# Performance work log

Hardware: AMD Instinct MI355X
Metric: run time of the kernel (lower is better)

## Reference

```python
import jax, jax.numpy as jnp
import numpy as np

N = 8192
H_DIM = 128
N_CLASSES = 10


def _cdist(a, b):
    # Euclidean distance matrix, torch.cdist(p=2) equivalent.
    d2 = (jnp.sum(a * a, axis=1)[:, None]
          + jnp.sum(b * b, axis=1)[None, :]
          - 2.0 * (a @ b.T))
    return jnp.sqrt(jnp.maximum(d2, 0.0))


def _adagae_regularization(distances, k):
    # Per-row sort-based adaptive-kernel thresholding (AdaGAE).
    sd = jnp.sort(distances, axis=1)            # [n, n]
    a = sd[:, k][:, None] + 1e-10               # k-th NN distance per row
    b = jnp.sum(sd[:, :k], axis=1)[:, None]     # sum of k nearest
    c = jax.nn.relu(a - distances)
    denom = a * k - b + 1e-10
    out = c / denom
    return (out + out.T) / 2.0


def _get_kernel(x, ohm_labels, sparsity):
    unknown = jnp.sum(ohm_labels, axis=1) == 0   # [n] bool
    known = ~unknown
    kk = known[:, None] & known[None, :]         # known-known region
    uu = unknown[:, None] & unknown[None, :]     # unknown-unknown region
    semantic = ohm_labels @ ohm_labels.T
    ed = _cdist(x, x)
    ed = (ed + ed.T) / 2.0
    adagae = _adagae_regularization(ed, sparsity)
    n_unknown = jnp.sum(unknown.astype(jnp.float32))
    fc = 1.0 / jnp.maximum(n_unknown, 1.0)       # heterogeneous fully-connected value
    kernel = jnp.where(kk, semantic, jnp.where(uu, adagae, fc))
    return kernel


def setup_inputs() -> dict:
    key = jax.random.key(0)
    k1, k2, k3 = jax.random.split(key, 3)
    x = jax.random.normal(k1, (N, H_DIM), dtype=jnp.float32)
    # labels in [0, N_CLASSES]; label == N_CLASSES -> unknown (all-zero one-hot row)
    labels = jax.random.randint(k2, (N,), 0, N_CLASSES + 1)
    ohm_labels = jnp.where((labels < N_CLASSES)[:, None],
                           jax.nn.one_hot(labels, N_CLASSES, dtype=jnp.float32),
                           0.0)
    W = jax.random.normal(k3, (2, H_DIM), dtype=jnp.float32) / np.sqrt(H_DIM)
    b = jnp.zeros((2,), dtype=jnp.float32)
    return {"x": x, "ohm_labels": ohm_labels, "W": W, "b": b, "spars": 32}


def reference(x, ohm_labels, W, b, spars):
    adj = _get_kernel(x, ohm_labels, spars)      # [n, n]
    h = x @ W.T + b                              # [n, 2]
    g = jnp.tanh(adj @ h)                        # [n, 2]
    # centroids (missing clusters stay zero)
    counts = jnp.sum(ohm_labels, axis=0)         # [n_classes]
    agg = ohm_labels.T @ g                       # [n_classes, 2]
    centroids = jnp.where((counts > 0)[:, None],
                          agg / jnp.maximum(counts, 1.0)[:, None], 0.0)
    scores = -_cdist(g, centroids)               # [n, n_classes]
    return scores, g, adj
```

## Files before the change

kernel.cpp:

```cpp
#include <hip/hip_runtime.h>
#include <hip/hip_bf16.h>
#include <math.h>

#define N 8192
#define D 128
#define NC 10

typedef float f4 __attribute__((ext_vector_type(4)));

__device__ __forceinline__ void nt_store4(float* p, float a, float b, float c, float d) {
    f4 v; v[0] = a; v[1] = b; v[2] = c; v[3] = d;
    __builtin_nontemporal_store(v, (f4*)p);
}


__global__ void k_zero(int* __restrict__ p) {
    if (threadIdx.x == 0) *p = 0;
}

__global__ void k_prep(const float* __restrict__ x, const float* __restrict__ ohm,
                       const float* __restrict__ W, const float* __restrict__ bb,
                       char* __restrict__ labs, float* __restrict__ nArr,
                       float* __restrict__ h, int* __restrict__ u_idx,
                       int* __restrict__ cpos, int* __restrict__ nuCnt) {
    int gt = blockIdx.x * blockDim.x + threadIdx.x;
    int wid = gt >> 6;
    int lane = gt & 63;
    if (wid >= N) return;
    const float2* xr = (const float2*)(x + (size_t)wid * D);
    float2 xv = xr[lane];
    float2 w0 = ((const float2*)W)[lane];
    float2 w1 = ((const float2*)(W + D))[lane];
    float nn = xv.x * xv.x + xv.y * xv.y;
    float h0 = xv.x * w0.x + xv.y * w0.y;
    float h1 = xv.x * w1.x + xv.y * w1.y;
    for (int off = 32; off; off >>= 1) {
        nn += __shfl_down(nn, off);
        h0 += __shfl_down(h0, off);
        h1 += __shfl_down(h1, off);
    }
    if (lane == 0) {
        nArr[wid] = nn;
        h[wid * 2 + 0] = h0 + bb[0];
        h[wid * 2 + 1] = h1 + bb[1];
        const float* orow = ohm + (size_t)wid * NC;
        int lab = -1;
        for (int c = 0; c < NC; ++c) {
            if (orow[c] > 0.5f) { lab = c; break; }
        }
        labs[wid] = (char)lab;
        if (lab < 0) {
            int slot = atomicAdd(nuCnt, 1);
            u_idx[slot] = wid;
            cpos[wid] = slot;
        }
    }
}

__global__ void k_sumA(const char* __restrict__ labs, const float* __restrict__ h,
                       float* __restrict__ part1) {
    __shared__ float L[256][33];
    int t = threadIdx.x;
    for (int s = 0; s < 33; ++s) L[t][s] = 0.f;
    int row = blockIdx.x * 256 + t;
    if (row < N) {
        int lab = labs[row];
        float h0 = h[row * 2], h1 = h[row * 2 + 1];
        if (lab >= 0) {
            L[t][lab * 2] = h0; L[t][lab * 2 + 1] = h1; L[t][22 + lab] = 1.f;
        } else {
            L[t][20] = h0; L[t][21] = h1; L[t][32] = 1.f;
        }
    }
    __syncthreads();
    if (t < 33) {
        float s = 0.f;
        for (int i = 0; i < 256; ++i) s += L[i][t];
        part1[blockIdx.x * 33 + t] = s;
    }
}

__global__ void k_sumB(const float* __restrict__ part1, float* __restrict__ scal) {
    int t = threadIdx.x;
    if (t < 33) {
        float s = 0.f;
        for (int i = 0; i < 64; ++i) s += part1[i * 33 + t];
        scal[t] = s;
    }
    __syncthreads();
    if (t == 0) {
        scal[33] = 1.0f / fmaxf(scal[32], 1.0f);
    }
}

__global__ void k_gemm(const float* __restrict__ x, const float* __restrict__ nArr,
                       const int* __restrict__ u_idx, const int* __restrict__ nuCnt,
                       int cap, float* __restrict__ d2a, float* __restrict__ adj) {
    __shared__ float As[64][132];
    __shared__ float Bs[64][132];
    __shared__ int Ai[64];
    int nu = *nuCnt;
    float* dst = (nu <= cap) ? d2a : adj;
    int t = threadIdx.x;
    int j0 = blockIdx.x * 64;
    for (int yy = blockIdx.y; yy * 64 < nu && yy < 128; yy += 12) {
        int a0 = yy * 64;
        if (yy != (int)blockIdx.y) __syncthreads();
        for (int c = t; c < 64 * 32; c += 256) {
            int r = c >> 5, c4 = c & 31;
            int a = a0 + r;
            int orig = (a < nu) ? u_idx[a] : u_idx[0];
            if (c4 == 0) Ai[r] = (a < nu) ? orig : -1;
            float4 av = ((const float4*)(x + (size_t)orig * D))[c4];
            *(float4*)&As[r][c4 * 4] = av;
            float4 bv = ((const float4*)(x + (size_t)(j0 + r) * D))[c4];
            *(float4*)&Bs[r][c4 * 4] = bv;
        }
        __syncthreads();
        int tx = t & 15, ty = t >> 4;
        float acc[4][4];
#pragma unroll
        for (int m = 0; m < 4; ++m)
#pragma unroll
            for (int q = 0; q < 4; ++q) acc[m][q] = 0.f;
#pragma unroll 4
        for (int k4 = 0; k4 < 32; ++k4) {
            float4 a4[4], b4[4];
#pragma unroll
            for (int m = 0; m < 4; ++m) a4[m] = *(const float4*)&As[ty + 16 * m][k4 * 4];
#pragma unroll
            for (int q = 0; q < 4; ++q) b4[q] = *(const float4*)&Bs[tx + 16 * q][k4 * 4];
#pragma unroll
            for (int m = 0; m < 4; ++m)
#pragma unroll
                for (int q = 0; q < 4; ++q)
                    acc[m][q] += a4[m].x * b4[q].x + a4[m].y * b4[q].y
                               + a4[m].z * b4[q].z + a4[m].w * b4[q].w;
        }
#pragma unroll
        for (int m = 0; m < 4; ++m) {
            int ar = ty + 16 * m;
            int orig = Ai[ar];
            if (orig < 0) continue;
            float ni = nArr[orig];
#pragma unroll
            for (int q = 0; q < 4; ++q) {
                int j = j0 + tx + 16 * q;
                float v = fmaxf(ni + nArr[j] - 2.f * acc[m][q], 0.f);
                if (orig == j) v = 0.f;
                dst[(size_t)(a0 + ar) * N + j] = v;
            }
        }
    }
}

__global__ void k_self(const float* __restrict__ d2a, const float* __restrict__ adj_ro,
                       const int* __restrict__ u_idx, const int* __restrict__ nuCnt,
                       int cap, const int* __restrict__ spars,
                       const char* __restrict__ labs,
                       float* __restrict__ aArr, float* __restrict__ dinv,
                       float* __restrict__ adj) {
    __shared__ float wsf[4];
    __shared__ int wsi[8];
    int nu = *nuCnt;
    int t = threadIdx.x;
    int bid = blockIdx.x;
    if (bid >= 1024) {
        if (nu > cap) return;
        float fc = 1.0f / fmaxf((float)nu, 1.0f);
        int fb = bid - 1024;
        for (int rr = 0; rr < 4; ++rr) {
            int i = fb + 2048 * rr;
            int li = labs[i];
            if (li < 0) continue;
            float* row = adj + (size_t)i * N;
#pragma unroll
            for (int s = 0; s < 8; ++s) {
                int c4 = t + 256 * s;
                char4 l4 = ((const char4*)labs)[c4];
                float o0 = (l4.x < 0) ? fc : ((l4.x == li) ? 1.f : 0.f);
                float o1 = (l4.y < 0) ? fc : ((l4.y == li) ? 1.f : 0.f);
                float o2 = (l4.z < 0) ? fc : ((l4.z == li) ? 1.f : 0.f);
                float o3 = (l4.w < 0) ? fc : ((l4.w == li) ? 1.f : 0.f);
                nt_store4(row + c4 * 4, o0, o1, o2, o3);
            }
        }
        return;
    }
    const float* src = (nu <= cap) ? d2a : adj_ro;
    int k = *spars;
    int need = k + 1;
    int w = t >> 6;
    for (int rr = 0; rr < 8; ++rr) {
        int a = bid + 1024 * rr;
        if (a >= nu) break;
        const float4* rp = (const float4*)(src + (size_t)a * N);
        float v[32];
#pragma unroll
        for (int s = 0; s < 8; ++s) {
            float4 q = rp[t + 256 * s];
            v[s * 4 + 0] = q.x; v[s * 4 + 1] = q.y; v[s * 4 + 2] = q.z; v[s * 4 + 3] = q.w;
        }
        unsigned lo = 0u, hi = 0x7F800000u;
        for (int it = 0; it < 32; ++it) {
            unsigned mid = (lo + hi) >> 1;
            float mf = __uint_as_float(mid);
            int c = 0;
#pragma unroll
            for (int s = 0; s < 32; ++s) c += (v[s] <= mf) ? 1 : 0;
            for (int off = 32; off; off >>= 1) c += __shfl_down(c, off);
            if ((t & 63) == 0) wsi[(it & 1) * 4 + w] = c;
            __syncthreads();
            int base = (it & 1) * 4;
            c = wsi[base] + wsi[base + 1] + wsi[base + 2] + wsi[base + 3];
            if (lo < hi) {
                if (c >= need) hi = mid; else lo = mid + 1;
            }
        }
        float kvf = __uint_as_float(hi);
        float sum = 0.f; int clt = 0;
#pragma unroll
        for (int s = 0; s < 32; ++s) {
            if (v[s] < kvf) { clt++; sum += sqrtf(v[s]); }
        }
        for (int off = 32; off; off >>= 1) {
            sum += __shfl_down(sum, off);
            clt += __shfl_down(clt, off);
        }
        __syncthreads();
        if ((t & 63) == 0) { wsf[w] = sum; wsi[w] = clt; }
        __syncthreads();
        if (t == 0) {
            float sAll = wsf[0] + wsf[1] + wsf[2] + wsf[3];
            int cAll = wsi[0] + wsi[1] + wsi[2] + wsi[3];
            float skv = sqrtf(kvf);
            float aV = skv + 1e-10f;
            float b = sAll + (float)(k - cAll) * skv;
            float denom = aV * (float)k - b + 1e-10f;
            int orig = u_idx[a];
            aArr[orig] = aV;
            dinv[orig] = 1.0f / denom;
        }
        __syncthreads();
    }
}

__global__ void k_fu(const float* __restrict__ d2a, const char* __restrict__ labs,
                     const int* __restrict__ u_idx, const float* __restrict__ aArr,
                     const float* __restrict__ dinv, const float* __restrict__ h,
                     const int* __restrict__ nuCnt, int cap,
                     float* __restrict__ adj, float* __restrict__ gp) {
    __shared__ float red[256];
    int nu = *nuCnt;
    if (nu > cap) return;
    int t = threadIdx.x;
    int jc = blockIdx.x;
    float fc = 1.0f / fmaxf((float)nu, 1.0f);
    const float2* h2 = (const float2*)h;
    for (int a = blockIdx.y; a < nu; a += 768) {
        int i = u_idx[a];
        float ai = aArr[i], di = dinv[i];
        const float* drow = d2a + (size_t)a * N;
        float* orow = adj + (size_t)i * N;
        float s0 = 0.f, s1 = 0.f;
#pragma unroll
        for (int s = 0; s < 2; ++s) {
            int c4 = jc * 512 + s * 256 + t;
            int j = c4 * 4;
            float4 dv = ((const float4*)drow)[c4];
            char4 l4 = ((const char4*)labs)[c4];
            float dd[4] = {dv.x, dv.y, dv.z, dv.w};
            signed char ll[4] = {(signed char)l4.x, (signed char)l4.y,
                                 (signed char)l4.z, (signed char)l4.w};
            float v[4];
#pragma unroll
            for (int q = 0; q < 4; ++q) {
                if (ll[q] >= 0) {
                    v[q] = fc;
                } else {
                    float d = sqrtf(dd[q]);
                    v[q] = 0.5f * (fmaxf(ai - d, 0.f) * di
                                 + fmaxf(aArr[j + q] - d, 0.f) * dinv[j + q]);
                }
                float2 hh = h2[j + q];
                s0 += v[q] * hh.x;
                s1 += v[q] * hh.y;
            }
            nt_store4(orow + j, v[0], v[1], v[2], v[3]);
        }
        red[t] = s0; __syncthreads();
        for (int off = 128; off; off >>= 1) {
            if (t < off) red[t] += red[t + off];
            __syncthreads();
        }
        float r0 = red[0];
        __syncthreads();
        red[t] = s1; __syncthreads();
        for (int off = 128; off; off >>= 1) {
            if (t < off) red[t] += red[t + off];
            __syncthreads();
        }
        if (t == 0) { gp[a * 8 + jc * 2 + 0] = r0; gp[a * 8 + jc * 2 + 1] = red[0]; }
        __syncthreads();
    }
}

__global__ void k_fill_known_fb(const char* __restrict__ labs,
                                const int* __restrict__ nuCnt, int cap,
                                float* __restrict__ adj) {
    int nu = *nuCnt;
    if (nu <= cap) return;
    int t = threadIdx.x;
    float fc = 1.0f / fmaxf((float)nu, 1.0f);
    for (int rr = 0; rr < 4; ++rr) {
        int i = blockIdx.x + 2048 * rr;
        int li = labs[i];
        if (li < 0) continue;
        float* row = adj + (size_t)i * N;
#pragma unroll
        for (int s = 0; s < 8; ++s) {
            int c4 = t + 256 * s;
            char4 l4 = ((const char4*)labs)[c4];
            float o0 = (l4.x < 0) ? fc : ((l4.x == li) ? 1.f : 0.f);
            float o1 = (l4.y < 0) ? fc : ((l4.y == li) ? 1.f : 0.f);
            float o2 = (l4.z < 0) ? fc : ((l4.z == li) ? 1.f : 0.f);
            float o3 = (l4.w < 0) ? fc : ((l4.w == li) ? 1.f : 0.f);
            nt_store4(row + c4 * 4, o0, o1, o2, o3);
        }
    }
}

__global__ void k_fu_slow(const float* __restrict__ x, const float* __restrict__ nArr,
                          const int* __restrict__ u_idx, const int* __restrict__ nuCnt,
                          int cap, const char* __restrict__ labs,
                          const float* __restrict__ aArr, const float* __restrict__ dinv,
                          float* __restrict__ adj) {
    __shared__ float As[64][D + 1];
    __shared__ float Bs[64][D + 1];
    __shared__ int Ai[64];
    int nu = *nuCnt;
    if (nu <= cap) return;
    int t = threadIdx.x;
    float fc = 1.0f / fmaxf((float)nu, 1.0f);
    int j0 = blockIdx.x * 64;
    for (int yy = blockIdx.y; yy * 64 < nu && yy < 128; yy += 12) {
        int a0 = yy * 64;
        if (yy != (int)blockIdx.y) __syncthreads();
        for (int c = t; c < 64 * 32; c += 256) {
            int r = c >> 5, c4 = c & 31;
            int a = a0 + r;
            int orig = (a < nu) ? u_idx[a] : u_idx[0];
            if (c4 == 0) Ai[r] = (a < nu) ? orig : -1;
            float4 av = ((const float4*)(x + (size_t)orig * D))[c4];
            As[r][c4 * 4 + 0] = av.x; As[r][c4 * 4 + 1] = av.y;
            As[r][c4 * 4 + 2] = av.z; As[r][c4 * 4 + 3] = av.w;
            float4 bv = ((const float4*)(x + (size_t)(j0 + r) * D))[c4];
            Bs[r][c4 * 4 + 0] = bv.x; Bs[r][c4 * 4 + 1] = bv.y;
            Bs[r][c4 * 4 + 2] = bv.z; Bs[r][c4 * 4 + 3] = bv.w;
        }
        __syncthreads();
        int tx = t & 15, ty = t >> 4;
        float acc[4][4];
#pragma unroll
        for (int m = 0; m < 4; ++m)
#pragma unroll
            for (int q = 0; q < 4; ++q) acc[m][q] = 0.f;
#pragma unroll 4
        for (int k = 0; k < D; ++k) {
            float a4[4], b4[4];
#pragma unroll
            for (int m = 0; m < 4; ++m) a4[m] = As[ty * 4 + m][k];
#pragma unroll
            for (int q = 0; q < 4; ++q) b4[q] = Bs[tx * 4 + q][k];
#pragma unroll
            for (int m = 0; m < 4; ++m)
#pragma unroll
                for (int q = 0; q < 4; ++q) acc[m][q] += a4[m] * b4[q];
        }
#pragma unroll
        for (int m = 0; m < 4; ++m) {
            int ar = ty * 4 + m;
            int orig = Ai[ar];
            if (orig < 0) continue;
            float ni = nArr[orig];
            float ai = aArr[orig], di = dinv[orig];
            int jb = j0 + tx * 4;
            float4 o;
            float* op = (float*)&o;
#pragma unroll
            for (int q = 0; q < 4; ++q) {
                int j = jb + q;
                int lj = labs[j];
                float v;
                if (lj >= 0) {
                    v = fc;
                } else {
                    float d2 = fmaxf(ni + nArr[j] - 2.f * acc[m][q], 0.f);
                    if (orig == j) d2 = 0.f;
                    float d = sqrtf(d2);
                    v = 0.5f * (fmaxf(ai - d, 0.f) * di + fmaxf(aArr[j] - d, 0.f) * dinv[j]);
                }
                op[q] = v;
            }
            *((float4*)(adj + (size_t)orig * N + jb)) = o;
        }
    }
}

__global__ void k_gv(const float* __restrict__ adj, const float* __restrict__ h,
                     const int* __restrict__ u_idx, const int* __restrict__ nuCnt,
                     int cap, float* __restrict__ gpre) {
    __shared__ float red[256];
    int nu = *nuCnt;
    if (nu <= cap) return;
    int t = threadIdx.x;
    const float2* h2 = (const float2*)h;
    for (int rr = 0; rr < 8; ++rr) {
        int a = blockIdx.x + 1024 * rr;
        if (a >= nu) break;
        int orig = u_idx[a];
        const float4* row = (const float4*)(adj + (size_t)orig * N);
        float s0 = 0.f, s1 = 0.f;
#pragma unroll
        for (int s = 0; s < 8; ++s) {
            int c4 = t + 256 * s;
            float4 v = row[c4];
            int j = c4 * 4;
            float2 ha = h2[j + 0], hb = h2[j + 1], hc = h2[j + 2], hd = h2[j + 3];
            s0 += v.x * ha.x + v.y * hb.x + v.z * hc.x + v.w * hd.x;
            s1 += v.x * ha.y + v.y * hb.y + v.z * hc.y + v.w * hd.y;
        }
        red[t] = s0; __syncthreads();
        for (int off = 128; off; off >>= 1) {
            if (t < off) red[t] += red[t + off];
            __syncthreads();
        }
        if (t == 0) gpre[orig * 2 + 0] = red[0];
        __syncthreads();
        red[t] = s1; __syncthreads();
        for (int off = 128; off; off >>= 1) {
            if (t < off) red[t] += red[t + off];
            __syncthreads();
        }
        if (t == 0) gpre[orig * 2 + 1] = red[0];
        __syncthreads();
    }
}

__global__ void k_gagg(const char* __restrict__ labs, const float* __restrict__ gp,
                       const float* __restrict__ gpre, const int* __restrict__ cpos,
                       const int* __restrict__ nuCnt, int cap,
                       const float* __restrict__ scal, float* __restrict__ outg,
                       float* __restrict__ part2) {
    __shared__ float L[256][21];
    int nu = *nuCnt;
    int t = threadIdx.x;
    for (int s = 0; s < 20; ++s) L[t][s] = 0.f;
    int i = blockIdx.x * 256 + t;
    int li = labs[i];
    float fc = scal[33];
    float g0, g1;
    if (li >= 0) {
        g0 = scal[li * 2 + 0] + fc * scal[20];
        g1 = scal[li * 2 + 1] + fc * scal[21];
    } else if (nu <= cap) {
        int a = cpos[i];
        g0 = gp[a * 8 + 0] + gp[a * 8 + 2] + gp[a * 8 + 4] + gp[a * 8 + 6];
        g1 = gp[a * 8 + 1] + gp[a * 8 + 3] + gp[a * 8 + 5] + gp[a * 8 + 7];
    } else {
        g0 = gpre[i * 2 + 0];
        g1 = gpre[i * 2 + 1];
    }
    g0 = tanhf(g0); g1 = tanhf(g1);
    outg[i * 2 + 0] = g0;
    outg[i * 2 + 1] = g1;
    if (li >= 0) { L[t][li * 2 + 0] = g0; L[t][li * 2 + 1] = g1; }
    __syncthreads();
    if (t < 20) {
        float s = 0.f;
        for (int r = 0; r < 256; ++r) s += L[r][t];
        part2[blockIdx.x * 20 + t] = s;
    }
}

__global__ void k_scores(const float* __restrict__ g, const float* __restrict__ part2,
                         const float* __restrict__ scal, float* __restrict__ outs) {
    __shared__ float cent[20];
    int t = threadIdx.x;
    if (t < 20) {
        float s = 0.f;
        for (int i = 0; i < 32; ++i) s += part2[i * 20 + t];
        float cnt = scal[22 + (t >> 1)];
        cent[t] = (cnt > 0.f) ? s / fmaxf(cnt, 1.0f) : 0.f;
    }
    __syncthreads();
    int i = blockIdx.x * 256 + t;
    float g0 = g[i * 2 + 0], g1 = g[i * 2 + 1];
#pragma unroll
    for (int c = 0; c < NC; ++c) {
        float d0 = g0 - cent[c * 2 + 0];
        float d1 = g1 - cent[c * 2 + 1];
        outs[i * NC + c] = -sqrtf(d0 * d0 + d1 * d1);
    }
}

extern "C" void kernel_launch(void* const* d_in, const int* in_sizes, int n_in,
                              void* d_out, int out_size, void* d_ws, size_t ws_size,
                              hipStream_t stream) {
    const float* x = (const float*)d_in[0];
    const float* ohm = (const float*)d_in[1];
    const float* W = (const float*)d_in[2];
    const float* b = (const float*)d_in[3];
    const int* spars = (const int*)d_in[4];

    float* out = (float*)d_out;
    float* outScores = out;
    float* outG = out + (size_t)N * NC;
    float* adj = outG + (size_t)N * 2;

    char* wsb = (char*)d_ws;
    int* u_idx   = (int*)(wsb + 0);
    char* labs   = (char*)(wsb + 32768);
    float* nArr  = (float*)(wsb + 40960);
    float* aArr  = (float*)(wsb + 73728);
    float* dinv  = (float*)(wsb + 106496);
    float* hArr  = (float*)(wsb + 139264);
    float* gpre  = (float*)(wsb + 204800);
    float* part1 = (float*)(wsb + 270336);
    float* part2 = (float*)(wsb + 278784);
    float* scal  = (float*)(wsb + 283904);
    int* nuCnt   = (int*)(wsb + 284160);
    int* cpos    = (int*)(wsb + 335872);
    float* gp    = (float*)(wsb + 524288);
    float* d2a   = (float*)(wsb + 2097152);

    long capL = ((long)ws_size - 2097152L) / ((long)N * 4);
    if (capL < 0) capL = 0;
    if (capL > N) capL = N;
    int cap = (int)capL;
    bool mayFallback = (cap < N);

    k_zero<<<1, 64, 0, stream>>>(nuCnt);
    k_prep<<<2048, 256, 0, stream>>>(x, ohm, W, b, labs, nArr, hArr, u_idx, cpos, nuCnt);
    k_sumA<<<64, 256, 0, stream>>>(labs, hArr, part1);
    k_sumB<<<1, 64, 0, stream>>>(part1, scal);
    k_gemm<<<dim3(128, 12), 256, 0, stream>>>(x, nArr, u_idx, nuCnt, cap, d2a, adj);
    k_self<<<3072, 256, 0, stream>>>(d2a, adj, u_idx, nuCnt, cap, spars, labs,
                                     aArr, dinv, adj);
    k_fu<<<dim3(4, 768), 256, 0, stream>>>(d2a, labs, u_idx, aArr, dinv, hArr,
                                           nuCnt, cap, adj, gp);
    if (mayFallback) {
        k_fill_known_fb<<<2048, 256, 0, stream>>>(labs, nuCnt, cap, adj);
        k_fu_slow<<<dim3(128, 12), 256, 0, stream>>>(x, nArr, u_idx, nuCnt, cap, labs,
                                                     aArr, dinv, adj);
        k_gv<<<1024, 256, 0, stream>>>(adj, hArr, u_idx, nuCnt, cap, gpre);
    }
    k_gagg<<<32, 256, 0, stream>>>(labs, gp, gpre, cpos, nuCnt, cap, scal, outG, part2);
    k_scores<<<32, 256, 0, stream>>>(outG, part2, scal, outScores);
}
```

Measured before the change: 142.7 us.

## Overlap known-row fill with distance GEMM, split K tiles, drop sumB kernel

Moves part of the known-row adjacency fill (rows below FSPLIT) into extra blocks of the distance GEMM kernel so the store-bound fill runs alongside compute-bound GEMM blocks. The rest of the fill stays in k_self, with fewer blocks. The GEMM now loads K in four 32-wide chunks, which shrinks shared memory per block and may raise occupancy, at the cost of more barriers. The single-block k_sumB launch is removed, and its reduction is recomputed inside k_gagg and k_scores from part1.

```diff
diff --git a/kernel.cpp b/kernel.cpp
--- a/kernel.cpp
+++ b/kernel.cpp
@@ -5,6 +5,7 @@
 #define N 8192
 #define D 128
 #define NC 10
+#define FSPLIT 2720
 
 typedef float f4 __attribute__((ext_vector_type(4)));
 
@@ -80,62 +81,74 @@
     }
 }
 
-__global__ void k_sumB(const float* __restrict__ part1, float* __restrict__ scal) {
-    int t = threadIdx.x;
-    if (t < 33) {
-        float s = 0.f;
-        for (int i = 0; i < 64; ++i) s += part1[i * 33 + t];
-        scal[t] = s;
-    }
-    __syncthreads();
-    if (t == 0) {
-        scal[33] = 1.0f / fmaxf(scal[32], 1.0f);
-    }
-}
-
-__global__ void k_gemm(const float* __restrict__ x, const float* __restrict__ nArr,
-                       const int* __restrict__ u_idx, const int* __restrict__ nuCnt,
-                       int cap, float* __restrict__ d2a, float* __restrict__ adj) {
-    __shared__ float As[64][132];
-    __shared__ float Bs[64][132];
+__global__ void k_gf(const float* __restrict__ x, const float* __restrict__ nArr,
+                     const int* __restrict__ u_idx, const int* __restrict__ nuCnt,
+                     int cap, const char* __restrict__ labs,
+                     float* __restrict__ d2a, float* __restrict__ adj) {
+    __shared__ float As[64][36];
+    __shared__ float Bs[64][36];
     __shared__ int Ai[64];
     int nu = *nuCnt;
+    int t = threadIdx.x;
+    int gy = blockIdx.y;
+    if (gy >= 12) {
+        if (nu > cap) return;
+        int i = (gy - 12) * 128 + blockIdx.x;
+        if (i >= FSPLIT) return;
+        int li = labs[i];
+        if (li < 0) return;
+        float fc = 1.0f / fmaxf((float)nu, 1.0f);
+        float* row = adj + (size_t)i * N;
+#pragma unroll
+        for (int s = 0; s < 8; ++s) {
+            int c4 = t + 256 * s;
+            char4 l4 = ((const char4*)labs)[c4];
+            float o0 = (l4.x < 0) ? fc : ((l4.x == li) ? 1.f : 0.f);
+            float o1 = (l4.y < 0) ? fc : ((l4.y == li) ? 1.f : 0.f);
+            float o2 = (l4.z < 0) ? fc : ((l4.z == li) ? 1.f : 0.f);
+            float o3 = (l4.w < 0) ? fc : ((l4.w == li) ? 1.f : 0.f);
+            nt_store4(row + c4 * 4, o0, o1, o2, o3);
+        }
+        return;
+    }
     float* dst = (nu <= cap) ? d2a : adj;
-    int t = threadIdx.x;
     int j0 = blockIdx.x * 64;
-    for (int yy = blockIdx.y; yy * 64 < nu && yy < 128; yy += 12) {
+    for (int yy = gy; yy * 64 < nu && yy < 128; yy += 12) {
         int a0 = yy * 64;
-        if (yy != (int)blockIdx.y) __syncthreads();
-        for (int c = t; c < 64 * 32; c += 256) {
-            int r = c >> 5, c4 = c & 31;
-            int a = a0 + r;
-            int orig = (a < nu) ? u_idx[a] : u_idx[0];
-            if (c4 == 0) Ai[r] = (a < nu) ? orig : -1;
-            float4 av = ((const float4*)(x + (size_t)orig * D))[c4];
-            *(float4*)&As[r][c4 * 4] = av;
-            float4 bv = ((const float4*)(x + (size_t)(j0 + r) * D))[c4];
-            *(float4*)&Bs[r][c4 * 4] = bv;
-        }
-        __syncthreads();
+        if (yy != gy) __syncthreads();
         int tx = t & 15, ty = t >> 4;
         float acc[4][4];
 #pragma unroll
         for (int m = 0; m < 4; ++m)
 #pragma unroll
             for (int q = 0; q < 4; ++q) acc[m][q] = 0.f;
+        for (int kh = 0; kh < 4; ++kh) {
+            if (kh) __syncthreads();
+            for (int c = t; c < 64 * 8; c += 256) {
+                int r = c >> 3, cc = c & 7;
+                int a = a0 + r;
+                int orig = (a < nu) ? u_idx[a] : u_idx[0];
+                if (kh == 0 && cc == 0) Ai[r] = (a < nu) ? orig : -1;
+                float4 av = ((const float4*)(x + (size_t)orig * D + kh * 32))[cc];
+                *(float4*)&As[r][cc * 4] = av;
+                float4 bv = ((const float4*)(x + (size_t)(j0 + r) * D + kh * 32))[cc];
+                *(float4*)&Bs[r][cc * 4] = bv;
+            }
+            __syncthreads();
 #pragma unroll 4
-        for (int k4 = 0; k4 < 32; ++k4) {
-            float4 a4[4], b4[4];
-#pragma unroll
-            for (int m = 0; m < 4; ++m) a4[m] = *(const float4*)&As[ty + 16 * m][k4 * 4];
-#pragma unroll
-            for (int q = 0; q < 4; ++q) b4[q] = *(const float4*)&Bs[tx + 16 * q][k4 * 4];
-#pragma unroll
-            for (int m = 0; m < 4; ++m)
-#pragma unroll
-                for (int q = 0; q < 4; ++q)
-                    acc[m][q] += a4[m].x * b4[q].x + a4[m].y * b4[q].y
-                               + a4[m].z * b4[q].z + a4[m].w * b4[q].w;
+            for (int k4 = 0; k4 < 8; ++k4) {
+                float4 a4[4], b4[4];
+#pragma unroll
+                for (int m = 0; m < 4; ++m) a4[m] = *(const float4*)&As[ty + 16 * m][k4 * 4];
+#pragma unroll
+                for (int q = 0; q < 4; ++q) b4[q] = *(const float4*)&Bs[tx + 16 * q][k4 * 4];
+#pragma unroll
+                for (int m = 0; m < 4; ++m)
+#pragma unroll
+                    for (int q = 0; q < 4; ++q)
+                        acc[m][q] += a4[m].x * b4[q].x + a4[m].y * b4[q].y
+                                   + a4[m].z * b4[q].z + a4[m].w * b4[q].w;
+            }
         }
 #pragma unroll
         for (int m = 0; m < 4; ++m) {
@@ -170,7 +183,8 @@
         float fc = 1.0f / fmaxf((float)nu, 1.0f);
         int fb = bid - 1024;
         for (int rr = 0; rr < 4; ++rr) {
-            int i = fb + 2048 * rr;
+            int i = FSPLIT + fb + 1368 * rr;
+            if (i >= N) break;
             int li = labs[i];
             if (li < 0) continue;
             float* row = adj + (size_t)i * N;
@@ -450,19 +464,26 @@
 __global__ void k_gagg(const char* __restrict__ labs, const float* __restrict__ gp,
                        const float* __restrict__ gpre, const int* __restrict__ cpos,
                        const int* __restrict__ nuCnt, int cap,
-                       const float* __restrict__ scal, float* __restrict__ outg,
+                       const float* __restrict__ part1, float* __restrict__ outg,
                        float* __restrict__ part2) {
     __shared__ float L[256][21];
+    __shared__ float sc[33];
     int nu = *nuCnt;
     int t = threadIdx.x;
     for (int s = 0; s < 20; ++s) L[t][s] = 0.f;
+    if (t < 33) {
+        float s = 0.f;
+        for (int i = 0; i < 64; ++i) s += part1[i * 33 + t];
+        sc[t] = s;
+    }
+    __syncthreads();
     int i = blockIdx.x * 256 + t;
     int li = labs[i];
-    float fc = scal[33];
+    float fc = 1.0f / fmaxf((float)nu, 1.0f);
     float g0, g1;
     if (li >= 0) {
-        g0 = scal[li * 2 + 0] + fc * scal[20];
-        g1 = scal[li * 2 + 1] + fc * scal[21];
+        g0 = sc[li * 2 + 0] + fc * sc[20];
+        g1 = sc[li * 2 + 1] + fc * sc[21];
     } else if (nu <= cap) {
         int a = cpos[i];
         g0 = gp[a * 8 + 0] + gp[a * 8 + 2] + gp[a * 8 + 4] + gp[a * 8 + 6];
@@ -484,13 +505,14 @@
 }
 
 __global__ void k_scores(const float* __restrict__ g, const float* __restrict__ part2,
-                         const float* __restrict__ scal, float* __restrict__ outs) {
+                         const float* __restrict__ part1, float* __restrict__ outs) {
     __shared__ float cent[20];
     int t = threadIdx.x;
     if (t < 20) {
         float s = 0.f;
         for (int i = 0; i < 32; ++i) s += part2[i * 20 + t];
-        float cnt = scal[22 + (t >> 1)];
+        float cnt = 0.f;
+        for (int i = 0; i < 64; ++i) cnt += part1[i * 33 + 22 + (t >> 1)];
         cent[t] = (cnt > 0.f) ? s / fmaxf(cnt, 1.0f) : 0.f;
     }
     __syncthreads();
@@ -528,7 +550,6 @@
     float* gpre  = (float*)(wsb + 204800);
     float* part1 = (float*)(wsb + 270336);
     float* part2 = (float*)(wsb + 278784);
-    float* scal  = (float*)(wsb + 283904);
     int* nuCnt   = (int*)(wsb + 284160);
     int* cpos    = (int*)(wsb + 335872);
     float* gp    = (float*)(wsb + 524288);
@@ -543,9 +564,8 @@
     k_zero<<<1, 64, 0, stream>>>(nuCnt);
     k_prep<<<2048, 256, 0, stream>>>(x, ohm, W, b, labs, nArr, hArr, u_idx, cpos, nuCnt);
     k_sumA<<<64, 256, 0, stream>>>(labs, hArr, part1);
-    k_sumB<<<1, 64, 0, stream>>>(part1, scal);
-    k_gemm<<<dim3(128, 12), 256, 0, stream>>>(x, nArr, u_idx, nuCnt, cap, d2a, adj);
-    k_self<<<3072, 256, 0, stream>>>(d2a, adj, u_idx, nuCnt, cap, spars, labs,
+    k_gf<<<dim3(128, 34), 256, 0, stream>>>(x, nArr, u_idx, nuCnt, cap, labs, d2a, adj);
+    k_self<<<2392, 256, 0, stream>>>(d2a, adj, u_idx, nuCnt, cap, spars, labs,
                                      aArr, dinv, adj);
     k_fu<<<dim3(4, 768), 256, 0, stream>>>(d2a, labs, u_idx, aArr, dinv, hArr,
                                            nuCnt, cap, adj, gp);
@@ -555,6 +575,6 @@
                                                      aArr, dinv, adj);
         k_gv<<<1024, 256, 0, stream>>>(adj, hArr, u_idx, nuCnt, cap, gpre);
     }
-    k_gagg<<<32, 256, 0, stream>>>(labs, gp, gpre, cpos, nuCnt, cap, scal, outG, part2);
-    k_scores<<<32, 256, 0, stream>>>(outG, part2, scal, outScores);
-}
+    k_gagg<<<32, 256, 0, stream>>>(labs, gp, gpre, cpos, nuCnt, cap, part1, outG, part2);
+    k_scores<<<32, 256, 0, stream>>>(outG, part2, part1, outScores);
+}
```

Measured after the change: 122.9 us. 13.9% less time.
